# Optimization experiments

Hardware: AMD Instinct MI355X
Metric: run time of the kernel (lower is better)

The kernel has to match this reference:

```python
import jax, jax.numpy as jnp
import numpy as np

# dims (see shape_source): emb_dim=256, input_size=256 -> d_model=1024
B, L = 8, 1024
QUES = 4000
EMB = 256
DM = 1024          # input_size + 768
DI = 2048          # expand * d_model
N = 16             # d_state
DTR = 64           # dt_rank = ceil(d_model/16)
K = 4              # d_conv
EPS = 1e-12


def setup_inputs() -> dict:
    key = jax.random.key(0)
    ks = jax.random.split(key, 16)
    s = 0.02
    nrm = lambda k, sh: jax.random.normal(k, sh, dtype=jnp.float32) * s
    return {
        "x": jax.random.randint(ks[0], (B, L), 0, 2 * QUES + 1),
        "q_id": jax.random.randint(ks[1], (B, L), 0, QUES),
        "emb_table": nrm(ks[2], (2 * QUES + 1, EMB)),
        "ques_cont": nrm(ks[3], (QUES, 768)),
        "ln0_g": jnp.ones((DM,), jnp.float32),
        "ln0_b": jnp.zeros((DM,), jnp.float32),
        "in_proj_w": nrm(ks[4], (2 * DI, DM)),
        "conv_w": nrm(ks[5], (DI, K)),
        "conv_b": jnp.zeros((DI,), jnp.float32),
        "x_proj_w": nrm(ks[6], (DTR + 2 * N, DI)),
        "dt_proj_w": nrm(ks[7], (DI, DTR)),
        "dt_proj_b": nrm(ks[8], (DI,)),
        "A_log": jnp.log(jax.random.uniform(ks[9], (DI, N), jnp.float32, 1.0, 16.0)),
        "D_param": jnp.ones((DI,), jnp.float32),
        "out_proj_w": nrm(ks[10], (DM, DI)),
        "ln1_g": jnp.ones((DM,), jnp.float32),
        "ln1_b": jnp.zeros((DM,), jnp.float32),
        "fc_w": nrm(ks[11], (QUES, DM)),
        "fc_b": jnp.zeros((QUES,), jnp.float32),
    }


def _ln(x, g, b):
    m = x.mean(-1, keepdims=True)
    v = ((x - m) ** 2).mean(-1, keepdims=True)
    return (x - m) / jnp.sqrt(v + EPS) * g + b


def _mamba(xm, in_proj_w, conv_w, conv_b, x_proj_w, dt_proj_w, dt_proj_b,
           A_log, D_param, out_proj_w):
    # xm: [B, L, DM]
    u_r = xm @ in_proj_w.T                           # [B, L, 2*DI]
    u, r = jnp.split(u_r, 2, axis=-1)                # each [B, L, DI]
    Lq = u.shape[1]
    # causal depthwise conv1d (padding=K-1, truncated to L)
    u_pad = jnp.pad(u, ((0, 0), (K - 1, 0), (0, 0)))
    conv = sum(u_pad[:, k:k + Lq, :] * conv_w[:, k] for k in range(K)) + conv_b
    u = jax.nn.silu(conv)
    dbl = u @ x_proj_w.T                             # [B, L, DTR+2N]
    dt, Bm, Cm = dbl[..., :DTR], dbl[..., DTR:DTR + N], dbl[..., DTR + N:]
    delta = jax.nn.softplus(dt @ dt_proj_w.T + dt_proj_b)   # [B, L, DI]
    A = -jnp.exp(A_log)                              # [DI, N]

    def step(h, ins):
        d_t, b_t, c_t, u_t = ins                     # [B,DI],[B,N],[B,N],[B,DI]
        dA = jnp.exp(d_t[:, :, None] * A)            # [B, DI, N]
        h = dA * h + d_t[:, :, None] * b_t[:, None, :] * u_t[:, :, None]
        y_t = jnp.einsum('bdn,bn->bd', h, c_t)
        return h, y_t

    xs = (delta.transpose(1, 0, 2), Bm.transpose(1, 0, 2),
          Cm.transpose(1, 0, 2), u.transpose(1, 0, 2))
    h0 = jnp.zeros((u.shape[0], DI, N), u.dtype)
    _, ys = jax.lax.scan(step, h0, xs)               # ys: [L, B, DI]
    y = ys.transpose(1, 0, 2) + u * D_param
    y = y * jax.nn.silu(r)
    return y @ out_proj_w.T                          # [B, L, DM]


def reference(x, q_id, emb_table, ques_cont, ln0_g, ln0_b, in_proj_w, conv_w,
              conv_b, x_proj_w, dt_proj_w, dt_proj_b, A_log, D_param,
              out_proj_w, ln1_g, ln1_b, fc_w, fc_b):
    x_e = emb_table[x]                               # [B, L, 256]
    x_c = ques_cont[q_id]                            # [B, L, 768]
    item = _ln(jnp.concatenate([x_e, x_c], axis=-1), ln0_g, ln0_b)
    # source loop applies every layer to item_emb; only the last layer's
    # output is used, so compute exactly that one layer (num_layers=2 branch).
    h = _mamba(item, in_proj_w, conv_w, conv_b, x_proj_w, dt_proj_w,
               dt_proj_b, A_log, D_param, out_proj_w)
    out = _ln(h + item, ln1_g, ln1_b)
    return jax.nn.sigmoid(out @ fc_w.T + fc_b)       # [B, L, QUES]
```

## Files before the change

kernel.cpp:

```cpp
#include <hip/hip_runtime.h>
#include <cstdint>
#include <cstddef>

#define L_SEQ 1024
#define BATCH 8
#define DMODEL 1024
#define DINNER 2048
#define NSTATE 16
#define DTRANK 64
#define NQ 4000
#define NROWS (BATCH * L_SEQ)
#define CH 32
#define NCH (L_SEQ / CH)

typedef float f32x4 __attribute__((ext_vector_type(4)));
typedef __bf16 bf16x8 __attribute__((ext_vector_type(8)));

#define AS1 __attribute__((address_space(1)))
#define AS3 __attribute__((address_space(3)))

__device__ __forceinline__ unsigned short f2bf(float f) {
  union { float f; unsigned int u; } c; c.f = f;
  unsigned int u = c.u;
  unsigned int r = u + 0x7fffu + ((u >> 16) & 1u);
  return (unsigned short)(r >> 16);
}

__device__ __forceinline__ float sigmoidf_(float x) { return 1.f / (1.f + expf(-x)); }

__global__ void cast_bf16_k(const float* __restrict__ src, unsigned short* __restrict__ dst, int n) {
  int i = blockIdx.x * blockDim.x + threadIdx.x;
  if (i < n) dst[i] = f2bf(src[i]);
}

__device__ __forceinline__ float blk_sum(float v, float* s) {
  #pragma unroll
  for (int o = 32; o > 0; o >>= 1) v += __shfl_down(v, o, 64);
  int w = threadIdx.x >> 6;
  if ((threadIdx.x & 63) == 0) s[w] = v;
  __syncthreads();
  float r = s[0] + s[1] + s[2] + s[3];
  __syncthreads();
  return r;
}

__global__ __launch_bounds__(256) void embed_ln0_k(
    const int* __restrict__ x, const int* __restrict__ qid,
    const float* __restrict__ emb, const float* __restrict__ qc,
    const float* __restrict__ g, const float* __restrict__ bta,
    float* __restrict__ item, unsigned short* __restrict__ item_bf)
{
  __shared__ float sbuf[4];
  int i = blockIdx.x;
  int t = threadIdx.x;
  float4 v;
  if (t < 64) v = *(const float4*)&emb[(size_t)x[i] * 256 + t * 4];
  else        v = *(const float4*)&qc[(size_t)qid[i] * 768 + t * 4 - 256];
  float tot = blk_sum(v.x + v.y + v.z + v.w, sbuf);
  float mean = tot * (1.f / 1024.f);
  float dx = v.x - mean, dy = v.y - mean, dz = v.z - mean, dw = v.w - mean;
  float var = blk_sum(dx*dx + dy*dy + dz*dz + dw*dw, sbuf) * (1.f / 1024.f);
  float rstd = rsqrtf(var + 1e-12f);
  float vals[4] = {dx, dy, dz, dw};
  size_t rb = (size_t)i * 1024;
  #pragma unroll
  for (int j = 0; j < 4; j++) {
    int c = t * 4 + j;
    float o = vals[j] * rstd * g[c] + bta[c];
    item[rb + c] = o;
    item_bf[rb + c] = f2bf(o);
  }
}

template <int EPI>
__global__ __launch_bounds__(256) void gemm_bt_k(
    const unsigned short* __restrict__ A, const unsigned short* __restrict__ Bw,
    float* __restrict__ C, const float* __restrict__ bias,
    int M, int N, int K)
{
  __shared__ __align__(16) unsigned short As[128 * 64];
  __shared__ __align__(16) unsigned short Bs[128 * 64];
  const int tid = threadIdx.x;
  const int m0 = blockIdx.x * 128;
  const int n0 = blockIdx.y * 128;
  const int w = tid >> 6, lane = tid & 63;
  const int wrow = (w >> 1) * 64, wcol = (w & 1) * 64;
  const int quad = lane >> 4, lid = lane & 15;

  const int srow = lane >> 3;
  const int schunk = (lane & 7) ^ srow;

  const unsigned short* Abase = A + (size_t)(m0 + w * 8 + srow) * K + schunk * 8;
  const unsigned short* Bbase[4];
  #pragma unroll
  for (int i = 0; i < 4; i++) {
    int rB = n0 + w * 8 + i * 32 + srow;
    if (rB > N - 1) rB = N - 1;
    Bbase[i] = Bw + (size_t)rB * K + schunk * 8;
  }

  f32x4 acc[4][4] = {};

  for (int k0 = 0; k0 < K; k0 += 64) {
    #pragma unroll
    for (int i = 0; i < 4; i++) {
      int rA = w * 8 + i * 32;
      __builtin_amdgcn_global_load_lds(
          (const AS1 unsigned int*)(Abase + (size_t)i * 32 * K + k0),
          (AS3 unsigned int*)&As[rA * 64], 16, 0, 0);
      __builtin_amdgcn_global_load_lds(
          (const AS1 unsigned int*)(Bbase[i] + k0),
          (AS3 unsigned int*)&Bs[rA * 64], 16, 0, 0);
    }
    __syncthreads();
    #pragma unroll
    for (int kk = 0; kk < 64; kk += 32) {
      bf16x8 af[4], bfr[4];
      #pragma unroll
      for (int mi = 0; mi < 4; mi++) {
        int r = wrow + mi * 16 + lid;
        int slot = ((kk >> 3) + quad) ^ (lid & 7);
        af[mi] = *(const bf16x8*)&As[r * 64 + slot * 8];
      }
      #pragma unroll
      for (int ni = 0; ni < 4; ni++) {
        int r = wcol + ni * 16 + lid;
        int slot = ((kk >> 3) + quad) ^ (lid & 7);
        bfr[ni] = *(const bf16x8*)&Bs[r * 64 + slot * 8];
      }
      #pragma unroll
      for (int mi = 0; mi < 4; mi++)
        #pragma unroll
        for (int ni = 0; ni < 4; ni++)
          acc[mi][ni] = __builtin_amdgcn_mfma_f32_16x16x32_bf16(af[mi], bfr[ni], acc[mi][ni], 0, 0, 0);
    }
    __syncthreads();
  }

  #pragma unroll
  for (int mi = 0; mi < 4; mi++) {
    #pragma unroll
    for (int ni = 0; ni < 4; ni++) {
      int col = n0 + wcol + ni * 16 + lid;
      if (col >= N) continue;
      #pragma unroll
      for (int r = 0; r < 4; r++) {
        int row = m0 + wrow + mi * 16 + quad * 4 + r;
        float v = acc[mi][ni][r];
        if (EPI == 1) v = sigmoidf_(v + bias[col]);
        C[(size_t)row * N + col] = v;
      }
    }
  }
}

__global__ void conv_silu_k(const float* __restrict__ u_r, const float* __restrict__ w,
                            const float* __restrict__ cb, float* __restrict__ uc,
                            unsigned short* __restrict__ uc_bf)
{
  int idx = blockIdx.x * blockDim.x + threadIdx.x;
  if (idx >= BATCH * L_SEQ * DINNER) return;
  int d = idx & (DINNER - 1);
  int l = (idx >> 11) & (L_SEQ - 1);
  int b = idx >> 21;
  float4 wv = ((const float4*)w)[d];
  size_t rb = ((size_t)b * L_SEQ + l) * (2 * DINNER) + d;
  float acc = cb[d];
  acc += wv.w * u_r[rb];
  if (l >= 1) acc += wv.z * u_r[rb - (2 * DINNER)];
  if (l >= 2) acc += wv.y * u_r[rb - 2 * (2 * DINNER)];
  if (l >= 3) acc += wv.x * u_r[rb - 3 * (2 * DINNER)];
  float s = acc * sigmoidf_(acc);
  uc[idx] = s;
  uc_bf[idx] = f2bf(s);
}

__global__ void dt_extract_k(const float* __restrict__ dbl, unsigned short* __restrict__ dt_bf)
{
  int i = blockIdx.x * blockDim.x + threadIdx.x;
  if (i >= NROWS * DTRANK) return;
  dt_bf[i] = f2bf(dbl[(size_t)(i >> 6) * 96 + (i & 63)]);
}

__global__ void softplus_k(float* dlt, const float* __restrict__ dtb)
{
  int i = blockIdx.x * blockDim.x + threadIdx.x;
  if (i >= NROWS * DINNER) return;
  float xx = dlt[i] + dtb[i & (DINNER - 1)];
  dlt[i] = fmaxf(xx, 0.f) + log1pf(expf(-fabsf(xx)));
}

__global__ void a2_k(const float* __restrict__ Alog, float* __restrict__ a2t)
{
  int i = blockIdx.x * blockDim.x + threadIdx.x;
  if (i >= DINNER * NSTATE) return;
  int d = i >> 4, n = i & 15;
  a2t[n * DINNER + d] = -expf(Alog[i]) * 1.4426950408889634f;
}

__global__ __launch_bounds__(64) void scan1_k(
    const float* __restrict__ dlt, const float* __restrict__ uc,
    const float* __restrict__ dbl, const float* __restrict__ a2t,
    float* __restrict__ Pbuf, float* __restrict__ Qbuf)
{
  int c = blockIdx.x;
  int dg = blockIdx.y;
  int b = blockIdx.z;
  int d = dg * 64 + threadIdx.x;
  float a2[NSTATE], P[NSTATE], q[NSTATE];
  #pragma unroll
  for (int n = 0; n < NSTATE; n++) {
    a2[n] = a2t[n * DINNER + d];
    P[n] = 1.f; q[n] = 0.f;
  }
  size_t base = ((size_t)(b * L_SEQ + c * CH)) * DINNER + d;
  const float* bc = dbl + (size_t)(b * L_SEQ + c * CH) * 96 + 64;
  for (int t = 0; t < CH; t++) {
    float dl = dlt[base];
    float du = dl * uc[base];
    #pragma unroll
    for (int n = 0; n < NSTATE; n++) {
      float dA = exp2f(dl * a2[n]);
      q[n] = dA * q[n] + du * bc[n];
      P[n] *= dA;
    }
    base += DINNER;
    bc += 96;
  }
  size_t ob = ((size_t)((b * NCH + c) * NSTATE)) * DINNER + d;
  #pragma unroll
  for (int n = 0; n < NSTATE; n++) {
    Pbuf[ob + (size_t)n * DINNER] = P[n];
    Qbuf[ob + (size_t)n * DINNER] = q[n];
  }
}

__global__ void scan_carry_k(const float* __restrict__ Pbuf, float* __restrict__ Qbuf)
{
  int idx = blockIdx.x * blockDim.x + threadIdx.x;
  if (idx >= BATCH * NSTATE * DINNER) return;
  int d = idx & (DINNER - 1);
  int n = (idx >> 11) & 15;
  int b = idx >> 15;
  float h = 0.f;
  for (int c = 0; c < NCH; c++) {
    size_t o = ((size_t)((b * NCH + c) * NSTATE + n)) * DINNER + d;
    float P = Pbuf[o];
    float q = Qbuf[o];
    Qbuf[o] = h;
    h = P * h + q;
  }
}

__global__ __launch_bounds__(64) void scan2_k(
    float* __restrict__ dlt,
    const float* __restrict__ uc,
    const float* __restrict__ dbl, const float* __restrict__ a2t,
    const float* __restrict__ Qbuf)
{
  int c = blockIdx.x;
  int dg = blockIdx.y;
  int b = blockIdx.z;
  int d = dg * 64 + threadIdx.x;
  float a2[NSTATE], h[NSTATE];
  size_t ob = ((size_t)((b * NCH + c) * NSTATE)) * DINNER + d;
  #pragma unroll
  for (int n = 0; n < NSTATE; n++) {
    a2[n] = a2t[n * DINNER + d];
    h[n] = Qbuf[ob + (size_t)n * DINNER];
  }
  size_t base = ((size_t)(b * L_SEQ + c * CH)) * DINNER + d;
  const float* bc = dbl + (size_t)(b * L_SEQ + c * CH) * 96 + 64;
  for (int t = 0; t < CH; t++) {
    float dl = dlt[base];
    float du = dl * uc[base];
    float yv = 0.f;
    #pragma unroll
    for (int n = 0; n < NSTATE; n++) {
      float dA = exp2f(dl * a2[n]);
      h[n] = dA * h[n] + du * bc[n];
      yv += h[n] * bc[NSTATE + n];
    }
    dlt[base] = yv;
    base += DINNER;
    bc += 96;
  }
}

__global__ void gate_k(const float* __restrict__ y, const float* __restrict__ uc,
                       const float* __restrict__ u_r, const float* __restrict__ Dp,
                       unsigned short* __restrict__ y_bf)
{
  int idx = blockIdx.x * blockDim.x + threadIdx.x;
  if (idx >= NROWS * DINNER) return;
  int d = idx & (DINNER - 1);
  int row = idx >> 11;
  float rv = u_r[(size_t)row * (2 * DINNER) + DINNER + d];
  float val = (y[idx] + uc[idx] * Dp[d]) * (rv * sigmoidf_(rv));
  y_bf[idx] = f2bf(val);
}

__global__ __launch_bounds__(256) void ln1_k(
    const float* __restrict__ mamba, const float* __restrict__ item,
    const float* __restrict__ g, const float* __restrict__ bta,
    unsigned short* __restrict__ out_bf)
{
  __shared__ float sbuf[4];
  int i = blockIdx.x;
  int t = threadIdx.x;
  size_t rb = (size_t)i * 1024 + t * 4;
  float4 v = *(const float4*)&mamba[rb];
  float4 w4 = *(const float4*)&item[rb];
  v.x += w4.x; v.y += w4.y; v.z += w4.z; v.w += w4.w;
  float tot = blk_sum(v.x + v.y + v.z + v.w, sbuf);
  float mean = tot * (1.f / 1024.f);
  float dx = v.x - mean, dy = v.y - mean, dz = v.z - mean, dw = v.w - mean;
  float var = blk_sum(dx*dx + dy*dy + dz*dz + dw*dw, sbuf) * (1.f / 1024.f);
  float rstd = rsqrtf(var + 1e-12f);
  float vals[4] = {dx, dy, dz, dw};
  #pragma unroll
  for (int j = 0; j < 4; j++) {
    int c = t * 4 + j;
    out_bf[(size_t)i * 1024 + c] = f2bf(vals[j] * rstd * g[c] + bta[c]);
  }
}

extern "C" void kernel_launch(void* const* d_in, const int* in_sizes, int n_in,
                              void* d_out, int out_size, void* d_ws, size_t ws_size,
                              hipStream_t stream)
{
  (void)in_sizes; (void)n_in; (void)out_size; (void)ws_size;
  const int*   x     = (const int*)d_in[0];
  const int*   qid   = (const int*)d_in[1];
  const float* emb   = (const float*)d_in[2];
  const float* qc    = (const float*)d_in[3];
  const float* ln0g  = (const float*)d_in[4];
  const float* ln0b  = (const float*)d_in[5];
  const float* w_in  = (const float*)d_in[6];
  const float* convw = (const float*)d_in[7];
  const float* convb = (const float*)d_in[8];
  const float* w_x   = (const float*)d_in[9];
  const float* w_dt  = (const float*)d_in[10];
  const float* dtb   = (const float*)d_in[11];
  const float* Alog  = (const float*)d_in[12];
  const float* Dp    = (const float*)d_in[13];
  const float* w_out = (const float*)d_in[14];
  const float* ln1g  = (const float*)d_in[15];
  const float* ln1b  = (const float*)d_in[16];
  const float* w_fc  = (const float*)d_in[17];
  const float* fcb   = (const float*)d_in[18];
  float* out = (float*)d_out;

  char* base = (char*)d_ws;
  size_t off = 0;
  auto carve = [&](size_t bytes) -> char* {
    char* p = base + off;
    off = (off + bytes + 255) & ~(size_t)255;
    return p;
  };
  float* item  = (float*)carve((size_t)NROWS * 1024 * 4);
  float* u_r   = (float*)carve((size_t)NROWS * 4096 * 4);
  float* uc    = (float*)carve((size_t)NROWS * 2048 * 4);
  float* dbl   = (float*)carve((size_t)NROWS * 96 * 4);
  float* dlt   = (float*)carve((size_t)NROWS * 2048 * 4);
  float* mamba = (float*)carve((size_t)NROWS * 1024 * 4);
  unsigned short* bfbuf  = (unsigned short*)carve((size_t)NROWS * 2048 * 2);
  unsigned short* bw_in  = (unsigned short*)carve((size_t)4096 * 1024 * 2);
  unsigned short* bw_x   = (unsigned short*)carve((size_t)96 * 2048 * 2);
  unsigned short* bw_dt  = (unsigned short*)carve((size_t)2048 * 64 * 2);
  unsigned short* bw_out = (unsigned short*)carve((size_t)1024 * 2048 * 2);
  unsigned short* bw_fc  = (unsigned short*)carve((size_t)4000 * 1024 * 2);
  float* a2t   = (float*)carve((size_t)DINNER * NSTATE * 4);

  float* Pbuf = mamba;
  float* Qbuf = (float*)bfbuf;

  auto cv = [&](const float* s, unsigned short* dst, int n) {
    cast_bf16_k<<<(n + 255) / 256, 256, 0, stream>>>(s, dst, n);
  };
  cv(w_in,  bw_in,  4096 * 1024);
  cv(w_x,   bw_x,   96 * 2048);
  cv(w_dt,  bw_dt,  2048 * 64);
  cv(w_out, bw_out, 1024 * 2048);
  cv(w_fc,  bw_fc,  4000 * 1024);
  a2_k<<<(DINNER * NSTATE + 255) / 256, 256, 0, stream>>>(Alog, a2t);

  embed_ln0_k<<<NROWS, 256, 0, stream>>>(x, qid, emb, qc, ln0g, ln0b, item, bfbuf);

  gemm_bt_k<0><<<dim3(64, 32), 256, 0, stream>>>(bfbuf, bw_in, u_r, nullptr, NROWS, 4096, 1024);

  conv_silu_k<<<(NROWS * DINNER) / 256, 256, 0, stream>>>(u_r, convw, convb, uc, bfbuf);

  gemm_bt_k<0><<<dim3(64, 1), 256, 0, stream>>>(bfbuf, bw_x, dbl, nullptr, NROWS, 96, 2048);

  dt_extract_k<<<(NROWS * DTRANK) / 256, 256, 0, stream>>>(dbl, bfbuf);

  gemm_bt_k<0><<<dim3(64, 16), 256, 0, stream>>>(bfbuf, bw_dt, dlt, nullptr, NROWS, 2048, 64);

  softplus_k<<<(NROWS * DINNER) / 256, 256, 0, stream>>>(dlt, dtb);

  scan1_k<<<dim3(NCH, 32, BATCH), 64, 0, stream>>>(dlt, uc, dbl, a2t, Pbuf, Qbuf);
  scan_carry_k<<<(BATCH * NSTATE * DINNER) / 256, 256, 0, stream>>>(Pbuf, Qbuf);
  scan2_k<<<dim3(NCH, 32, BATCH), 64, 0, stream>>>(dlt, uc, dbl, a2t, Qbuf);

  gate_k<<<(NROWS * DINNER) / 256, 256, 0, stream>>>(dlt, uc, u_r, Dp, bfbuf);

  gemm_bt_k<0><<<dim3(64, 8), 256, 0, stream>>>(bfbuf, bw_out, mamba, nullptr, NROWS, 1024, 2048);

  ln1_k<<<NROWS, 256, 0, stream>>>(mamba, item, ln1g, ln1b, bfbuf);

  gemm_bt_k<1><<<dim3(64, 32), 256, 0, stream>>>(bfbuf, bw_fc, out, fcb, NROWS, 4000, 1024);
}
```

Measured before the change: 882.5 us.

## Add 256x256 double-buffered GEMM and fuse dt extract, softplus, gating into neighbors

Adds a 512-thread GEMM with 256x256 tiles, double-buffered direct global-to-LDS loads and a grouped block-index swizzle, and uses it for the in_proj and fc GEMMs. The dt bf16 extraction moves into the x_proj GEMM epilogue, softplus into the dt_proj GEMM epilogue, and the D-skip and SiLU gating into scan2, which now writes bf16 directly. This removes three elementwise kernels and their full-size memory round trips. Buffers are re-aliased (mamba holds dt_bf, y_bf and Pbuf; u_r holds the out_proj result), so correctness depends on lifetimes not overlapping.

```diff
diff --git a/kernel.cpp b/kernel.cpp
--- a/kernel.cpp
+++ b/kernel.cpp
@@ -76,6 +76,7 @@
 __global__ __launch_bounds__(256) void gemm_bt_k(
     const unsigned short* __restrict__ A, const unsigned short* __restrict__ Bw,
     float* __restrict__ C, const float* __restrict__ bias,
+    unsigned short* __restrict__ aux,
     int M, int N, int K)
 {
   __shared__ __align__(16) unsigned short As[128 * 64];
@@ -139,6 +140,110 @@
 
   #pragma unroll
   for (int mi = 0; mi < 4; mi++) {
+    #pragma unroll
+    for (int ni = 0; ni < 4; ni++) {
+      int col = n0 + wcol + ni * 16 + lid;
+      if (col >= N) continue;
+      #pragma unroll
+      for (int r = 0; r < 4; r++) {
+        int row = m0 + wrow + mi * 16 + quad * 4 + r;
+        float v = acc[mi][ni][r];
+        if (EPI == 1) v = sigmoidf_(v + bias[col]);
+        if (EPI == 2) { float xx = v + bias[col]; v = fmaxf(xx, 0.f) + log1pf(expf(-fabsf(xx))); }
+        C[(size_t)row * N + col] = v;
+        if (EPI == 3 && col < 64) aux[(size_t)row * 64 + col] = f2bf(v);
+      }
+    }
+  }
+}
+
+template <int EPI>
+__global__ __launch_bounds__(512, 2) void gemm256_k(
+    const unsigned short* __restrict__ A, const unsigned short* __restrict__ Bw,
+    float* __restrict__ C, const float* __restrict__ bias,
+    int M, int N, int K)
+{
+  __shared__ __align__(16) unsigned short As[2][256 * 64];
+  __shared__ __align__(16) unsigned short Bs[2][256 * 64];
+  const int tid = threadIdx.x;
+
+  const int gx = gridDim.x;
+  const int nwg = gx * gridDim.y;
+  int bid = blockIdx.y * gx + blockIdx.x;
+  if ((nwg & 7) == 0) bid = (bid & 7) * (nwg >> 3) + (bid >> 3);
+  const int m0 = (bid % gx) * 256;
+  const int n0 = (bid / gx) * 256;
+
+  const int w = tid >> 6, lane = tid & 63;
+  const int wrow = (w >> 2) * 128;
+  const int wcol = (w & 3) * 64;
+  const int quad = lane >> 4, lid = lane & 15;
+
+  const int srow = lane >> 3;
+  const int schunk = (lane & 7) ^ srow;
+
+  const unsigned short* Ab = A + (size_t)(m0 + w * 8 + srow) * K + schunk * 8;
+  const unsigned short* Bb[4];
+  #pragma unroll
+  for (int i = 0; i < 4; i++) {
+    int rB = n0 + w * 8 + i * 64 + srow;
+    if (rB > N - 1) rB = N - 1;
+    Bb[i] = Bw + (size_t)rB * K + schunk * 8;
+  }
+
+  f32x4 acc[8][4] = {};
+
+  auto stage = [&](int buf, int k0) {
+    #pragma unroll
+    for (int i = 0; i < 4; i++) {
+      int rg = (i * 64 + w * 8) * 64;
+      __builtin_amdgcn_global_load_lds(
+          (const AS1 unsigned int*)(Ab + (size_t)i * 64 * K + k0),
+          (AS3 unsigned int*)&As[buf][rg], 16, 0, 0);
+      __builtin_amdgcn_global_load_lds(
+          (const AS1 unsigned int*)(Bb[i] + k0),
+          (AS3 unsigned int*)&Bs[buf][rg], 16, 0, 0);
+    }
+  };
+
+  const int nt = K >> 6;
+  stage(0, 0);
+  __syncthreads();
+
+  for (int kt = 0; kt < nt; ++kt) {
+    const int cur = kt & 1;
+    if (kt + 1 < nt) stage(cur ^ 1, (kt + 1) << 6);
+
+    bf16x8 bfr[4][2];
+    #pragma unroll
+    for (int ni = 0; ni < 4; ni++) {
+      #pragma unroll
+      for (int kk2 = 0; kk2 < 2; kk2++) {
+        int r = wcol + ni * 16 + lid;
+        int slot = (kk2 * 4 + quad) ^ (lid & 7);
+        bfr[ni][kk2] = *(const bf16x8*)&Bs[cur][r * 64 + slot * 8];
+      }
+    }
+    #pragma unroll
+    for (int mi = 0; mi < 8; mi++) {
+      bf16x8 af[2];
+      #pragma unroll
+      for (int kk2 = 0; kk2 < 2; kk2++) {
+        int r = wrow + mi * 16 + lid;
+        int slot = (kk2 * 4 + quad) ^ (lid & 7);
+        af[kk2] = *(const bf16x8*)&As[cur][r * 64 + slot * 8];
+      }
+      #pragma unroll
+      for (int ni = 0; ni < 4; ni++) {
+        acc[mi][ni] = __builtin_amdgcn_mfma_f32_16x16x32_bf16(af[0], bfr[ni][0], acc[mi][ni], 0, 0, 0);
+        acc[mi][ni] = __builtin_amdgcn_mfma_f32_16x16x32_bf16(af[1], bfr[ni][1], acc[mi][ni], 0, 0, 0);
+      }
+    }
+    __syncthreads();
+  }
+
+  #pragma unroll
+  for (int mi = 0; mi < 8; mi++) {
     #pragma unroll
     for (int ni = 0; ni < 4; ni++) {
       int col = n0 + wcol + ni * 16 + lid;
@@ -175,21 +280,6 @@
   uc_bf[idx] = f2bf(s);
 }
 
-__global__ void dt_extract_k(const float* __restrict__ dbl, unsigned short* __restrict__ dt_bf)
-{
-  int i = blockIdx.x * blockDim.x + threadIdx.x;
-  if (i >= NROWS * DTRANK) return;
-  dt_bf[i] = f2bf(dbl[(size_t)(i >> 6) * 96 + (i & 63)]);
-}
-
-__global__ void softplus_k(float* dlt, const float* __restrict__ dtb)
-{
-  int i = blockIdx.x * blockDim.x + threadIdx.x;
-  if (i >= NROWS * DINNER) return;
-  float xx = dlt[i] + dtb[i & (DINNER - 1)];
-  dlt[i] = fmaxf(xx, 0.f) + log1pf(expf(-fabsf(xx)));
-}
-
 __global__ void a2_k(const float* __restrict__ Alog, float* __restrict__ a2t)
 {
   int i = blockIdx.x * blockDim.x + threadIdx.x;
@@ -253,10 +343,10 @@
 }
 
 __global__ __launch_bounds__(64) void scan2_k(
-    float* __restrict__ dlt,
-    const float* __restrict__ uc,
+    const float* __restrict__ dlt, const float* __restrict__ uc,
     const float* __restrict__ dbl, const float* __restrict__ a2t,
-    const float* __restrict__ Qbuf)
+    const float* __restrict__ Qbuf, const float* __restrict__ u_r,
+    const float* __restrict__ Dp, unsigned short* __restrict__ ybf)
 {
   int c = blockIdx.x;
   int dg = blockIdx.y;
@@ -269,11 +359,14 @@
     a2[n] = a2t[n * DINNER + d];
     h[n] = Qbuf[ob + (size_t)n * DINNER];
   }
+  float Dd = Dp[d];
   size_t base = ((size_t)(b * L_SEQ + c * CH)) * DINNER + d;
   const float* bc = dbl + (size_t)(b * L_SEQ + c * CH) * 96 + 64;
+  const float* rp = u_r + (size_t)(b * L_SEQ + c * CH) * (2 * DINNER) + DINNER + d;
   for (int t = 0; t < CH; t++) {
     float dl = dlt[base];
-    float du = dl * uc[base];
+    float uval = uc[base];
+    float du = dl * uval;
     float yv = 0.f;
     #pragma unroll
     for (int n = 0; n < NSTATE; n++) {
@@ -281,23 +374,13 @@
       h[n] = dA * h[n] + du * bc[n];
       yv += h[n] * bc[NSTATE + n];
     }
-    dlt[base] = yv;
+    float rv = *rp;
+    float val = (yv + uval * Dd) * (rv * sigmoidf_(rv));
+    ybf[base] = f2bf(val);
     base += DINNER;
     bc += 96;
-  }
-}
-
-__global__ void gate_k(const float* __restrict__ y, const float* __restrict__ uc,
-                       const float* __restrict__ u_r, const float* __restrict__ Dp,
-                       unsigned short* __restrict__ y_bf)
-{
-  int idx = blockIdx.x * blockDim.x + threadIdx.x;
-  if (idx >= NROWS * DINNER) return;
-  int d = idx & (DINNER - 1);
-  int row = idx >> 11;
-  float rv = u_r[(size_t)row * (2 * DINNER) + DINNER + d];
-  float val = (y[idx] + uc[idx] * Dp[d]) * (rv * sigmoidf_(rv));
-  y_bf[idx] = f2bf(val);
+    rp += 2 * DINNER;
+  }
 }
 
 __global__ __launch_bounds__(256) void ln1_k(
@@ -372,8 +455,11 @@
   unsigned short* bw_fc  = (unsigned short*)carve((size_t)4000 * 1024 * 2);
   float* a2t   = (float*)carve((size_t)DINNER * NSTATE * 4);
 
+  unsigned short* dt_bf = (unsigned short*)mamba;
   float* Pbuf = mamba;
   float* Qbuf = (float*)bfbuf;
+  unsigned short* y_bf = (unsigned short*)mamba;
+  float* mamba_out = u_r;
 
   auto cv = [&](const float* s, unsigned short* dst, int n) {
     cast_bf16_k<<<(n + 255) / 256, 256, 0, stream>>>(s, dst, n);
@@ -387,27 +473,21 @@
 
   embed_ln0_k<<<NROWS, 256, 0, stream>>>(x, qid, emb, qc, ln0g, ln0b, item, bfbuf);
 
-  gemm_bt_k<0><<<dim3(64, 32), 256, 0, stream>>>(bfbuf, bw_in, u_r, nullptr, NROWS, 4096, 1024);
+  gemm256_k<0><<<dim3(32, 16), 512, 0, stream>>>(bfbuf, bw_in, u_r, nullptr, NROWS, 4096, 1024);
 
   conv_silu_k<<<(NROWS * DINNER) / 256, 256, 0, stream>>>(u_r, convw, convb, uc, bfbuf);
 
-  gemm_bt_k<0><<<dim3(64, 1), 256, 0, stream>>>(bfbuf, bw_x, dbl, nullptr, NROWS, 96, 2048);
-
-  dt_extract_k<<<(NROWS * DTRANK) / 256, 256, 0, stream>>>(dbl, bfbuf);
-
-  gemm_bt_k<0><<<dim3(64, 16), 256, 0, stream>>>(bfbuf, bw_dt, dlt, nullptr, NROWS, 2048, 64);
-
-  softplus_k<<<(NROWS * DINNER) / 256, 256, 0, stream>>>(dlt, dtb);
+  gemm_bt_k<3><<<dim3(64, 1), 256, 0, stream>>>(bfbuf, bw_x, dbl, nullptr, dt_bf, NROWS, 96, 2048);
+
+  gemm_bt_k<2><<<dim3(64, 16), 256, 0, stream>>>(dt_bf, bw_dt, dlt, dtb, nullptr, NROWS, 2048, 64);
 
   scan1_k<<<dim3(NCH, 32, BATCH), 64, 0, stream>>>(dlt, uc, dbl, a2t, Pbuf, Qbuf);
   scan_carry_k<<<(BATCH * NSTATE * DINNER) / 256, 256, 0, stream>>>(Pbuf, Qbuf);
-  scan2_k<<<dim3(NCH, 32, BATCH), 64, 0, stream>>>(dlt, uc, dbl, a2t, Qbuf);
-
-  gate_k<<<(NROWS * DINNER) / 256, 256, 0, stream>>>(dlt, uc, u_r, Dp, bfbuf);
-
-  gemm_bt_k<0><<<dim3(64, 8), 256, 0, stream>>>(bfbuf, bw_out, mamba, nullptr, NROWS, 1024, 2048);
-
-  ln1_k<<<NROWS, 256, 0, stream>>>(mamba, item, ln1g, ln1b, bfbuf);
-
-  gemm_bt_k<1><<<dim3(64, 32), 256, 0, stream>>>(bfbuf, bw_fc, out, fcb, NROWS, 4000, 1024);
-}
+  scan2_k<<<dim3(NCH, 32, BATCH), 64, 0, stream>>>(dlt, uc, dbl, a2t, Qbuf, u_r, Dp, y_bf);
+
+  gemm_bt_k<0><<<dim3(64, 8), 256, 0, stream>>>(y_bf, bw_out, mamba_out, nullptr, nullptr, NROWS, 1024, 2048);
+
+  ln1_k<<<NROWS, 256, 0, stream>>>(mamba_out, item, ln1g, ln1b, bfbuf);
+
+  gemm256_k<1><<<dim3(32, 16), 512, 0, stream>>>(bfbuf, bw_fc, out, fcb, NROWS, 4000, 1024);
+}
```

New measurement: 861.5 us. 1.02x faster.
